# Kernel optimization log

Hardware: AMD Instinct MI355X
Metric: run time of the kernel (lower is better)

Reference implementation:

```python
import jax, jax.numpy as jnp
import numpy as np

IOU_THRESH = 0.5
NEG_POS_RATIO = 3
VAR0, VAR1 = 0.1, 0.2  # BoxCoder variances


def box_iou(a, b):
    # a: [G,4] xyxy, b: [P,4] xyxy -> [G,P]
    lt = jnp.maximum(a[:, None, :2], b[None, :, :2])
    rb = jnp.minimum(a[:, None, 2:], b[None, :, 2:])
    wh = jnp.clip(rb - lt, 0.0)
    inter = wh[..., 0] * wh[..., 1]
    area_a = (a[:, 2] - a[:, 0]) * (a[:, 3] - a[:, 1])
    area_b = (b[:, 2] - b[:, 0]) * (b[:, 3] - b[:, 1])
    return inter / (area_a[:, None] + area_b[None, :] - inter)


def xywha_to_xyxy(p):
    c, wh = p[:, :2], p[:, 2:]
    return jnp.concatenate([c - wh * 0.5, c + wh * 0.5], axis=-1)


def assign_targets(gt_boxes, gt_labels, priors_xyxy):
    # gt_boxes [G,4], gt_labels [G], priors_xyxy [P,4]
    iou = box_iou(gt_boxes, priors_xyxy)            # [G,P]
    matched_vals = iou.max(axis=0)                  # [P]
    matches = iou.argmax(axis=0)                    # [P]
    best_prior = iou.argmax(axis=1)                 # [G] best prior per target
    G = gt_boxes.shape[0]
    matches = matches.at[best_prior].set(jnp.arange(G))
    matched_vals = matched_vals.at[best_prior].set(2.0)
    labels = jnp.where(matched_vals < IOU_THRESH, 0, gt_labels[matches])  # [P]
    boxes = gt_boxes[matches]                       # [P,4]
    return boxes, labels


def encode(boxes_xyxy, priors_xywha):
    # SSD center-form encoding with variances
    ctr = (boxes_xyxy[:, :2] + boxes_xyxy[:, 2:]) * 0.5
    wh = boxes_xyxy[:, 2:] - boxes_xyxy[:, :2]
    g_c = (ctr - priors_xywha[:, :2]) / (VAR0 * priors_xywha[:, 2:])
    g_wh = jnp.log(wh / priors_xywha[:, 2:]) / VAR1
    return jnp.concatenate([g_c, g_wh], axis=-1)


def hard_negative_mask(bg_loss, labels):
    # bg_loss [B,P]: -log_softmax(logits)[...,0]; keep all positives and
    # top-(ratio*num_pos) hardest negatives per image.
    pos = labels > 0
    num_neg = pos.sum(axis=1, keepdims=True) * NEG_POS_RATIO
    loss = jnp.where(pos, -jnp.inf, bg_loss)
    order = jnp.argsort(-loss, axis=1)
    rank = jnp.argsort(order, axis=1)
    return pos | (rank < num_neg)


def reference(priors, class_logits, box_regression, gt_boxes, gt_labels):
    priors_xyxy = xywha_to_xyxy(priors)
    boxes, labels = jax.vmap(assign_targets, in_axes=(0, 0, None))(
        gt_boxes, gt_labels, priors_xyxy)            # [B,P,4], [B,P]
    regression_targets = jax.vmap(encode, in_axes=(0, None))(boxes, priors)

    logp = jax.nn.log_softmax(class_logits, axis=-1)  # [B,P,C]
    bg_loss = jax.lax.stop_gradient(-logp[..., 0])
    mask = hard_negative_mask(bg_loss, labels)        # [B,P] bool

    # masked cross-entropy, reduction='sum'
    ce = -jnp.take_along_axis(logp, labels[..., None], axis=-1)[..., 0]
    loss_classifier = jnp.sum(jnp.where(mask, ce, 0.0))

    # masked smooth-L1 (beta=1), reduction='sum' over positives
    pos = labels > 0
    d = jnp.abs(box_regression - regression_targets)
    sl1 = jnp.where(d < 1.0, 0.5 * d * d, d - 0.5)
    loss_box_reg = jnp.sum(jnp.where(pos[..., None], sl1, 0.0))

    num_pos = jnp.sum(pos).astype(class_logits.dtype)
    return loss_box_reg / num_pos, loss_classifier / num_pos


def setup_inputs() -> dict:
    key = jax.random.key(0)
    ks = jax.random.split(key, 8)
    B, P, C, G = 64, 8732, 81, 16
    # priors: xywha in [0,1] with small positive wh
    p_c = jax.random.uniform(ks[0], (P, 2), jnp.float32, 0.05, 0.95)
    p_wh = jax.random.uniform(ks[1], (P, 2), jnp.float32, 0.02, 0.25)
    priors = jnp.concatenate([p_c, p_wh], axis=-1)
    class_logits = jax.random.normal(ks[2], (B, P, C), jnp.float32)
    box_regression = jax.random.normal(ks[3], (B, P, 4), jnp.float32)
    # gt boxes: valid xyxy in [0,1] with positive size
    g_c = jax.random.uniform(ks[4], (B, G, 2), jnp.float32, 0.2, 0.8)
    g_wh = jax.random.uniform(ks[5], (B, G, 2), jnp.float32, 0.05, 0.3)
    gt_boxes = jnp.concatenate([g_c - g_wh * 0.5, g_c + g_wh * 0.5], axis=-1)
    gt_labels = jax.random.randint(ks[6], (B, G), 1, C, jnp.int32)
    return {"priors": priors, "class_logits": class_logits,
            "box_regression": box_regression, "gt_boxes": gt_boxes,
            "gt_labels": gt_labels}
```

## Files before the change

kernel.cpp:

```cpp
#include <hip/hip_runtime.h>
#include <cfloat>

#define GT 16
#define NCLS 81
#define TPB 256
#define MAXP 8732
#define TROWS 64
#define WF4 324
#define TF4 (TROWS*NCLS/4)

__device__ __forceinline__ float smoothl1(float d){
  float a = fabsf(d);
  return a < 1.0f ? 0.5f*a*a : a - 0.5f;
}

__global__ __launch_bounds__(TPB) void assign1(
    const float* __restrict__ priors,
    const float* __restrict__ gt_boxes,
    long long* __restrict__ best,
    float* __restrict__ mvv,
    unsigned char* __restrict__ mmatch,
    float* __restrict__ ce_pos, float* __restrict__ sl1_sum,
    int* __restrict__ num_pos, float* __restrict__ out,
    int P)
{
  const int b = blockIdx.x >> 3, chunk = blockIdx.x & 7;
  const int CH = (P + 7) >> 3;
  const int p0 = chunk*CH, p1 = min(p0 + CH, P);
  const int tid = threadIdx.x, wave = tid >> 6, lane = tid & 63;
  if (chunk == 0 && tid == 0){ ce_pos[b] = 0.0f; sl1_sum[b] = 0.0f; num_pos[b] = 0; }
  if (blockIdx.x == 0 && tid < 2) out[tid] = 0.0f;
  __shared__ float gx0[GT], gy0[GT], gx1[GT], gy1[GT], ga[GT];
  __shared__ float redv[4*GT]; __shared__ int redi[4*GT];
  if (tid < GT){
    const float4 gb = ((const float4*)gt_boxes)[b*GT + tid];
    gx0[tid]=gb.x; gy0[tid]=gb.y; gx1[tid]=gb.z; gy1[tid]=gb.w;
    ga[tid] = (gb.z-gb.x)*(gb.w-gb.y);
  }
  __syncthreads();
  float bv[GT]; int bi[GT];
  #pragma unroll
  for (int g=0; g<GT; ++g){ bv[g] = -1.0f; bi[g] = 0x7fffffff; }
  for (int p = p0 + tid; p < p1; p += TPB){
    const float4 pr = ((const float4*)priors)[p];
    const float px0 = pr.x - pr.z*0.5f, py0 = pr.y - pr.w*0.5f;
    const float px1 = pr.x + pr.z*0.5f, py1 = pr.y + pr.w*0.5f;
    const float pa = (px1-px0)*(py1-py0);
    float mv = -1.0f; int mi = 0;
    #pragma unroll
    for (int g=0; g<GT; ++g){
      const float w = fmaxf(fminf(gx1[g],px1) - fmaxf(gx0[g],px0), 0.0f);
      const float h = fmaxf(fminf(gy1[g],py1) - fmaxf(gy0[g],py0), 0.0f);
      const float inter = w*h;
      const float iou = inter / (ga[g] + pa - inter);
      if (iou > mv){ mv = iou; mi = g; }
      if (iou > bv[g]){ bv[g] = iou; bi[g] = p; }
    }
    mvv[(long long)b*P + p] = mv;
    mmatch[(long long)b*P + p] = (unsigned char)mi;
  }
  #pragma unroll
  for (int g=0; g<GT; ++g){
    float v = bv[g]; int i = bi[g];
    for (int off=32; off>0; off>>=1){
      const float ov = __shfl_down(v, off);
      const int   oi = __shfl_down(i, off);
      if (ov > v || (ov == v && oi < i)){ v = ov; i = oi; }
    }
    if (lane == 0){ redv[wave*GT+g] = v; redi[wave*GT+g] = i; }
  }
  __syncthreads();
  if (tid < GT){
    float v = redv[tid]; int i = redi[tid];
    for (int w=1; w<4; ++w){
      const float ov = redv[w*GT+tid]; const int oi = redi[w*GT+tid];
      if (ov > v || (ov == v && oi < i)){ v = ov; i = oi; }
    }
    const long long pk =
      ((long long)(unsigned long long)__float_as_uint(v) << 32)
      | (long long)(0xFFFFFFFFu - (unsigned)i);
    atomicMax(&best[b*GT + tid], pk);
  }
}

__global__ __launch_bounds__(TPB) void assign2(
    const float* __restrict__ priors,
    const float* __restrict__ gt_boxes,
    const int*   __restrict__ gt_labels,
    const float* __restrict__ box_reg,
    const long long* __restrict__ best,
    const float* __restrict__ mvv,
    const unsigned char* __restrict__ mmatch,
    int*   __restrict__ labels_out,
    float* __restrict__ sl1_sum,
    int*   __restrict__ num_pos,
    int P)
{
  const int b = blockIdx.x >> 3, chunk = blockIdx.x & 7;
  const int CH = (P + 7) >> 3;
  const int p0 = chunk*CH, p1 = min(p0 + CH, P);
  const int tid = threadIdx.x, wave = tid >> 6, lane = tid & 63;
  __shared__ float gx0[GT], gy0[GT], gx1[GT], gy1[GT];
  __shared__ int glab[GT], bp[GT];
  __shared__ float rs[4]; __shared__ int rc[4];
  if (tid < GT){
    const float4 gb = ((const float4*)gt_boxes)[b*GT + tid];
    gx0[tid]=gb.x; gy0[tid]=gb.y; gx1[tid]=gb.z; gy1[tid]=gb.w;
    glab[tid] = gt_labels[b*GT + tid];
    bp[tid] = (int)(0xFFFFFFFFu - (unsigned)((unsigned long long)best[b*GT + tid] & 0xFFFFFFFFull));
  }
  __syncthreads();
  float sl1 = 0.0f; int cnt = 0;
  for (int p = p0 + tid; p < p1; p += TPB){
    float mv = mvv[(long long)b*P + p];
    int g = mmatch[(long long)b*P + p];
    #pragma unroll
    for (int g2=0; g2<GT; ++g2) if (bp[g2] == p){ mv = 2.0f; g = g2; }
    int lab = 0;
    if (mv >= 0.5f){
      lab = glab[g]; cnt++;
      const float4 pr = ((const float4*)priors)[p];
      const float ctrx = (gx0[g]+gx1[g])*0.5f, ctry = (gy0[g]+gy1[g])*0.5f;
      const float wx = gx1[g]-gx0[g], wy = gy1[g]-gy0[g];
      const float tx = (ctrx - pr.x) / (0.1f*pr.z);
      const float ty = (ctry - pr.y) / (0.1f*pr.w);
      const float tw = __logf(wx/pr.z) / 0.2f;
      const float th = __logf(wy/pr.w) / 0.2f;
      const float4 br = ((const float4*)box_reg)[(long long)b*P + p];
      sl1 += smoothl1(br.x - tx) + smoothl1(br.y - ty)
           + smoothl1(br.z - tw) + smoothl1(br.w - th);
    }
    labels_out[(long long)b*P + p] = lab;
  }
  float v = sl1; int c = cnt;
  for (int off=32; off>0; off>>=1){ v += __shfl_down(v, off); c += __shfl_down(c, off); }
  if (lane == 0){ rs[wave] = v; rc[wave] = c; }
  __syncthreads();
  if (tid == 0){
    atomicAdd(&sl1_sum[b], rs[0]+rs[1]+rs[2]+rs[3]);
    atomicAdd(&num_pos[b], rc[0]+rc[1]+rc[2]+rc[3]);
  }
}

__global__ __launch_bounds__(TPB) void lse_pipe(
    const float* __restrict__ logits,
    const int*   __restrict__ labels,
    float* __restrict__ bg,
    float* __restrict__ ce_pos,
    int P, int NT)
{
  __shared__ float s[TROWS*NCLS];
  const int tid = threadIdx.x;
  const int wave = tid >> 6, lane = tid & 63;
  const int rl = lane >> 2, q = lane & 3;
  const int c0 = q ? (1+20*q) : 0;
  const int c1 = 21 + 20*q;
  const int G = gridDim.x;
  int t = blockIdx.x;
  if (t >= NT) return;

  float4 r0,r1,r2,r3,r4,r5; int labc = 0;
  {
    const float4* src = (const float4*)logits + (long long)t*TF4 + wave*WF4;
    r0 = src[lane]; r1 = src[lane+64]; r2 = src[lane+128];
    r3 = src[lane+192]; r4 = src[lane+256];
    if (lane < 4) r5 = src[lane+320];
    if (q == 0) labc = labels[t*TROWS + wave*16 + rl];
  }
  float4* sd = (float4*)(s) + wave*WF4;
  const float* x = s + wave*(WF4*4) + rl*NCLS;
  for (; t < NT; t += G){
    sd[lane] = r0; sd[lane+64] = r1; sd[lane+128] = r2;
    sd[lane+192] = r3; sd[lane+256] = r4;
    if (lane < 4) sd[lane+320] = r5;
    const int lab = labc;
    const int tn = t + G;
    if (tn < NT){
      const float4* src = (const float4*)logits + (long long)tn*TF4 + wave*WF4;
      r0 = src[lane]; r1 = src[lane+64]; r2 = src[lane+128];
      r3 = src[lane+192]; r4 = src[lane+256];
      if (lane < 4) r5 = src[lane+320];
      if (q == 0) labc = labels[tn*TROWS + wave*16 + rl];
    }
    float sum = 0.0f;
    for (int c = c0; c < c1; ++c) sum += __expf(x[c]);
    sum += __shfl_xor(sum, 1);
    sum += __shfl_xor(sum, 2);
    if (q == 0){
      const int row = t*TROWS + wave*16 + rl;
      const float lse = __logf(sum);
      float bgv;
      if (lab > 0){
        const int b = row / P;
        const float xl = x[lab];
        atomicAdd(&ce_pos[b], lse - xl);
        bgv = 0.0f;
      } else {
        bgv = fmaxf(lse - x[0], 0.0f);
      }
      bg[row] = bgv;
    }
  }
}

__global__ __launch_bounds__(TPB) void topk_kernel(
    const float* __restrict__ bg,
    const int*   __restrict__ num_pos,
    const float* __restrict__ sl1_sum,
    const float* __restrict__ ce_pos,
    float* __restrict__ out,
    int P, int B)
{
  const int b = blockIdx.x;
  const int tid = threadIdx.x;
  const int wave = tid >> 6, lane = tid & 63;
  const int rep = tid & 15;
  __shared__ float sv[MAXP];
  __shared__ unsigned cntR[16][257];
  __shared__ unsigned s_wc[4];
  __shared__ float    s_wf[4];
  __shared__ unsigned s_prefix;
  __shared__ int s_krem, s_chosen, s_newk;

  {
    const float4* srcp = (const float4*)(bg + (long long)b * P);
    float4* dst = (float4*)sv;
    for (int j = tid; j < P/4; j += TPB) dst[j] = srcp[j];
  }
  if (tid == 0){
    const int k = 3*num_pos[b];
    s_krem = k < P ? k : P-1;
    s_prefix = 0u;
  }
  __syncthreads();

  for (int level=0; level<4; ++level){
    const int shift = 24 - 8*level;
    for (int i = tid; i < 16*257; i += TPB) ((unsigned*)cntR)[i] = 0u;
    __syncthreads();
    const unsigned pref = s_prefix;
    const int k = s_krem;
    for (int j = tid; j < P/4; j += TPB){
      const float4 f4 = ((const float4*)sv)[j];
      #pragma unroll
      for (int e=0; e<4; ++e){
        const unsigned key = __float_as_uint((&f4.x)[e]);
        const bool ok = (level == 0) || ((key >> (shift+8)) == pref);
        if (ok) atomicAdd(&cntR[rep][(key >> shift) & 255u], 1u);
      }
    }
    __syncthreads();
    const int rb = 255 - tid;
    unsigned c = 0;
    #pragma unroll
    for (int r=0; r<16; ++r) c += cntR[r][rb];
    unsigned cv = c;
    #pragma unroll
    for (int off=1; off<64; off<<=1){
      const unsigned oc = __shfl_up(cv, off);
      if (lane >= off) cv += oc;
    }
    if (lane == 63) s_wc[wave] = cv;
    __syncthreads();
    unsigned addc = 0;
    for (int w=0; w<4; ++w) if (w < wave) addc += s_wc[w];
    const unsigned S = cv - c + addc;
    if ((int)S <= k && k < (int)(S + c)){
      s_chosen = rb; s_newk = k - (int)S;
    }
    __syncthreads();
    if (tid == 0){
      s_krem = s_newk;
      s_prefix = (pref << 8) | (unsigned)s_chosen;
    }
    __syncthreads();
  }
  const unsigned T = s_prefix;
  float acc = 0.0f;
  for (int j = tid; j < P/4; j += TPB){
    const float4 f4 = ((const float4*)sv)[j];
    #pragma unroll
    for (int e=0; e<4; ++e){
      const float f = (&f4.x)[e];
      if (__float_as_uint(f) > T) acc += f;
    }
  }
  for (int off=32; off>0; off>>=1) acc += __shfl_down(acc, off);
  if (lane == 0) s_wf[wave] = acc;
  __syncthreads();
  if (tid < 64){
    float n = 0.0f;
    for (int i = tid; i < B; i += 64) n += (float)num_pos[i];
    for (int off=32; off>0; off>>=1) n += __shfl_down(n, off);
    if (tid == 0){
      const float N = n;
      const float cls = s_wf[0]+s_wf[1]+s_wf[2]+s_wf[3]
                      + (float)s_krem * __uint_as_float(T);
      atomicAdd(&out[0], sl1_sum[b] / N);
      atomicAdd(&out[1], (ce_pos[b] + cls) / N);
    }
  }
}

extern "C" void kernel_launch(void* const* d_in, const int* in_sizes, int n_in,
                              void* d_out, int out_size, void* d_ws, size_t ws_size,
                              hipStream_t stream) {
  const float* priors = (const float*)d_in[0];
  const float* logits = (const float*)d_in[1];
  const float* boxreg = (const float*)d_in[2];
  const float* gtb    = (const float*)d_in[3];
  const int*   gtl    = (const int*)d_in[4];
  const int P = in_sizes[0] / 4;
  const int B = in_sizes[4] / GT;
  const long long BP = (long long)B * P;

  char* ws = (char*)d_ws;
  int*   labels = (int*)ws;
  float* bgmv   = (float*)(ws + BP*4);
  unsigned char* mmatch = (unsigned char*)(ws + BP*8);
  char* tail = ws + BP*9;
  long long* best = (long long*)tail;
  float* sl1_s  = (float*)(tail + (long long)B*GT*8);
  int*   npos   = (int*)  (tail + (long long)B*GT*8 + 256);
  float* ce_pos = (float*)(tail + (long long)B*GT*8 + 512);

  assign1<<<B*8, TPB, 0, stream>>>(priors, gtb, best, bgmv, mmatch,
                                   ce_pos, sl1_s, npos, (float*)d_out, P);
  assign2<<<B*8, TPB, 0, stream>>>(priors, gtb, gtl, boxreg, best, bgmv, mmatch,
                                   labels, sl1_s, npos, P);
  const int NT = (int)(BP / TROWS);
  const int G = 1792;
  lse_pipe<<<G, TPB, 0, stream>>>(logits, labels, bgmv, ce_pos, P, NT);
  topk_kernel<<<B, TPB, 0, stream>>>(bgmv, npos, sl1_s, ce_pos, (float*)d_out, P, B);
}
```

Before: 340.6 us.

## Fuse target assignment into one per-image kernel with LDS-resident match state

Merges the two assignment kernels into a single kernel with one block per image. Per-prior max IoU and match index stay in shared memory (about 44KB), so the global scratch round-trip and the 64-bit atomicMax for the best prior go away. Labels are stored as bytes instead of ints. The LSE loop now uses a strided, unrolled class split across the four lanes of each row. The cost is that the assignment stage runs on only 64 blocks, cutting its parallelism eightfold, and the large shared-memory footprint limits occupancy.

```diff
diff --git a/kernel.cpp b/kernel.cpp
--- a/kernel.cpp
+++ b/kernel.cpp
@@ -14,34 +14,42 @@
   return a < 1.0f ? 0.5f*a*a : a - 0.5f;
 }
 
-__global__ __launch_bounds__(TPB) void assign1(
+__global__ __launch_bounds__(TPB) void assign_kernel(
     const float* __restrict__ priors,
     const float* __restrict__ gt_boxes,
-    long long* __restrict__ best,
-    float* __restrict__ mvv,
-    unsigned char* __restrict__ mmatch,
-    float* __restrict__ ce_pos, float* __restrict__ sl1_sum,
-    int* __restrict__ num_pos, float* __restrict__ out,
+    const int*   __restrict__ gt_labels,
+    const float* __restrict__ box_reg,
+    unsigned char* __restrict__ labels_out,
+    float* __restrict__ sl1_sum,
+    int*   __restrict__ num_pos,
+    float* __restrict__ ce_pos,
+    float* __restrict__ out,
     int P)
 {
-  const int b = blockIdx.x >> 3, chunk = blockIdx.x & 7;
-  const int CH = (P + 7) >> 3;
-  const int p0 = chunk*CH, p1 = min(p0 + CH, P);
+  const int b = blockIdx.x;
   const int tid = threadIdx.x, wave = tid >> 6, lane = tid & 63;
-  if (chunk == 0 && tid == 0){ ce_pos[b] = 0.0f; sl1_sum[b] = 0.0f; num_pos[b] = 0; }
-  if (blockIdx.x == 0 && tid < 2) out[tid] = 0.0f;
+
+  __shared__ float s_mv[MAXP];
+  __shared__ unsigned char s_match[MAXP];
   __shared__ float gx0[GT], gy0[GT], gx1[GT], gy1[GT], ga[GT];
+  __shared__ int glab[GT], bp[GT];
   __shared__ float redv[4*GT]; __shared__ int redi[4*GT];
+  __shared__ float rs[4]; __shared__ int rc[4];
+
+  if (tid == 0) ce_pos[b] = 0.0f;
+  if (b == 0 && tid < 2) out[tid] = 0.0f;
   if (tid < GT){
     const float4 gb = ((const float4*)gt_boxes)[b*GT + tid];
     gx0[tid]=gb.x; gy0[tid]=gb.y; gx1[tid]=gb.z; gy1[tid]=gb.w;
     ga[tid] = (gb.z-gb.x)*(gb.w-gb.y);
-  }
-  __syncthreads();
+    glab[tid] = gt_labels[b*GT + tid];
+  }
+  __syncthreads();
+
   float bv[GT]; int bi[GT];
   #pragma unroll
   for (int g=0; g<GT; ++g){ bv[g] = -1.0f; bi[g] = 0x7fffffff; }
-  for (int p = p0 + tid; p < p1; p += TPB){
+  for (int p = tid; p < P; p += TPB){
     const float4 pr = ((const float4*)priors)[p];
     const float px0 = pr.x - pr.z*0.5f, py0 = pr.y - pr.w*0.5f;
     const float px1 = pr.x + pr.z*0.5f, py1 = pr.y + pr.w*0.5f;
@@ -56,8 +64,8 @@
       if (iou > mv){ mv = iou; mi = g; }
       if (iou > bv[g]){ bv[g] = iou; bi[g] = p; }
     }
-    mvv[(long long)b*P + p] = mv;
-    mmatch[(long long)b*P + p] = (unsigned char)mi;
+    s_mv[p] = mv;
+    s_match[p] = (unsigned char)mi;
   }
   #pragma unroll
   for (int g=0; g<GT; ++g){
@@ -76,44 +84,14 @@
       const float ov = redv[w*GT+tid]; const int oi = redi[w*GT+tid];
       if (ov > v || (ov == v && oi < i)){ v = ov; i = oi; }
     }
-    const long long pk =
-      ((long long)(unsigned long long)__float_as_uint(v) << 32)
-      | (long long)(0xFFFFFFFFu - (unsigned)i);
-    atomicMax(&best[b*GT + tid], pk);
-  }
-}
-
-__global__ __launch_bounds__(TPB) void assign2(
-    const float* __restrict__ priors,
-    const float* __restrict__ gt_boxes,
-    const int*   __restrict__ gt_labels,
-    const float* __restrict__ box_reg,
-    const long long* __restrict__ best,
-    const float* __restrict__ mvv,
-    const unsigned char* __restrict__ mmatch,
-    int*   __restrict__ labels_out,
-    float* __restrict__ sl1_sum,
-    int*   __restrict__ num_pos,
-    int P)
-{
-  const int b = blockIdx.x >> 3, chunk = blockIdx.x & 7;
-  const int CH = (P + 7) >> 3;
-  const int p0 = chunk*CH, p1 = min(p0 + CH, P);
-  const int tid = threadIdx.x, wave = tid >> 6, lane = tid & 63;
-  __shared__ float gx0[GT], gy0[GT], gx1[GT], gy1[GT];
-  __shared__ int glab[GT], bp[GT];
-  __shared__ float rs[4]; __shared__ int rc[4];
-  if (tid < GT){
-    const float4 gb = ((const float4*)gt_boxes)[b*GT + tid];
-    gx0[tid]=gb.x; gy0[tid]=gb.y; gx1[tid]=gb.z; gy1[tid]=gb.w;
-    glab[tid] = gt_labels[b*GT + tid];
-    bp[tid] = (int)(0xFFFFFFFFu - (unsigned)((unsigned long long)best[b*GT + tid] & 0xFFFFFFFFull));
-  }
-  __syncthreads();
+    bp[tid] = i;
+  }
+  __syncthreads();
+
   float sl1 = 0.0f; int cnt = 0;
-  for (int p = p0 + tid; p < p1; p += TPB){
-    float mv = mvv[(long long)b*P + p];
-    int g = mmatch[(long long)b*P + p];
+  for (int p = tid; p < P; p += TPB){
+    float mv = s_mv[p];
+    int g = s_match[p];
     #pragma unroll
     for (int g2=0; g2<GT; ++g2) if (bp[g2] == p){ mv = 2.0f; g = g2; }
     int lab = 0;
@@ -130,21 +108,21 @@
       sl1 += smoothl1(br.x - tx) + smoothl1(br.y - ty)
            + smoothl1(br.z - tw) + smoothl1(br.w - th);
     }
-    labels_out[(long long)b*P + p] = lab;
+    labels_out[(long long)b*P + p] = (unsigned char)lab;
   }
   float v = sl1; int c = cnt;
   for (int off=32; off>0; off>>=1){ v += __shfl_down(v, off); c += __shfl_down(c, off); }
   if (lane == 0){ rs[wave] = v; rc[wave] = c; }
   __syncthreads();
   if (tid == 0){
-    atomicAdd(&sl1_sum[b], rs[0]+rs[1]+rs[2]+rs[3]);
-    atomicAdd(&num_pos[b], rc[0]+rc[1]+rc[2]+rc[3]);
+    sl1_sum[b] = rs[0]+rs[1]+rs[2]+rs[3];
+    num_pos[b] = rc[0]+rc[1]+rc[2]+rc[3];
   }
 }
 
 __global__ __launch_bounds__(TPB) void lse_pipe(
     const float* __restrict__ logits,
-    const int*   __restrict__ labels,
+    const unsigned char* __restrict__ labels,
     float* __restrict__ bg,
     float* __restrict__ ce_pos,
     int P, int NT)
@@ -153,8 +131,6 @@
   const int tid = threadIdx.x;
   const int wave = tid >> 6, lane = tid & 63;
   const int rl = lane >> 2, q = lane & 3;
-  const int c0 = q ? (1+20*q) : 0;
-  const int c1 = 21 + 20*q;
   const int G = gridDim.x;
   int t = blockIdx.x;
   if (t >= NT) return;
@@ -183,7 +159,10 @@
       if (q == 0) labc = labels[tn*TROWS + wave*16 + rl];
     }
     float sum = 0.0f;
-    for (int c = c0; c < c1; ++c) sum += __expf(x[c]);
+    #pragma unroll
+    for (int i = 0; i < 20; ++i) sum += __expf(x[q + 4*i]);
+    float x0 = 0.0f;
+    if (q == 0){ x0 = x[0]; sum += __expf(x[80]); }
     sum += __shfl_xor(sum, 1);
     sum += __shfl_xor(sum, 2);
     if (q == 0){
@@ -196,7 +175,7 @@
         atomicAdd(&ce_pos[b], lse - xl);
         bgv = 0.0f;
       } else {
-        bgv = fmaxf(lse - x[0], 0.0f);
+        bgv = fmaxf(lse - x0, 0.0f);
       }
       bg[row] = bgv;
     }
@@ -315,21 +294,18 @@
   const long long BP = (long long)B * P;
 
   char* ws = (char*)d_ws;
-  int*   labels = (int*)ws;
-  float* bgmv   = (float*)(ws + BP*4);
-  unsigned char* mmatch = (unsigned char*)(ws + BP*8);
-  char* tail = ws + BP*9;
-  long long* best = (long long*)tail;
-  float* sl1_s  = (float*)(tail + (long long)B*GT*8);
-  int*   npos   = (int*)  (tail + (long long)B*GT*8 + 256);
-  float* ce_pos = (float*)(tail + (long long)B*GT*8 + 512);
-
-  assign1<<<B*8, TPB, 0, stream>>>(priors, gtb, best, bgmv, mmatch,
-                                   ce_pos, sl1_s, npos, (float*)d_out, P);
-  assign2<<<B*8, TPB, 0, stream>>>(priors, gtb, gtl, boxreg, best, bgmv, mmatch,
-                                   labels, sl1_s, npos, P);
+  unsigned char* labels = (unsigned char*)ws;
+  float* bg     = (float*)(ws + BP);
+  char* tail = ws + BP*5;
+  float* sl1_s  = (float*)(tail);
+  int*   npos   = (int*)  (tail + 256);
+  float* ce_pos = (float*)(tail + 512);
+
+  assign_kernel<<<B, TPB, 0, stream>>>(priors, gtb, gtl, boxreg,
+                                       labels, sl1_s, npos, ce_pos,
+                                       (float*)d_out, P);
   const int NT = (int)(BP / TROWS);
   const int G = 1792;
-  lse_pipe<<<G, TPB, 0, stream>>>(logits, labels, bgmv, ce_pos, P, NT);
-  topk_kernel<<<B, TPB, 0, stream>>>(bgmv, npos, sl1_s, ce_pos, (float*)d_out, P, B);
-}
+  lse_pipe<<<G, TPB, 0, stream>>>(logits, labels, bg, ce_pos, P, NT);
+  topk_kernel<<<B, TPB, 0, stream>>>(bg, npos, sl1_s, ce_pos, (float*)d_out, P, B);
+}
```

Measured after the change: 387.7 us. 1.14x slower.
